# Performance work log

Hardware: AMD Instinct MI355X
Metric: run time of the kernel (lower is better)

The kernel has to match this reference:

```python
import jax, jax.numpy as jnp
import numpy as np

B, S, H, D = 4, 4096, 1024, 64

def setup_inputs() -> dict:
    key = jax.random.key(0)
    ks = jax.random.split(key, 10)
    return {
        "query": jax.random.normal(ks[0], (B, S, H), jnp.float32),
        "key": jax.random.normal(ks[1], (B, S, H), jnp.float32),
        "value": jax.random.normal(ks[2], (B, S, H), jnp.float32),
        "mask": jax.random.randint(ks[3], (B, S), 0, 2, jnp.int32),
        "Wq": jax.random.normal(ks[4], (H, D), jnp.float32) * 0.02,
        "bq": jax.random.normal(ks[5], (D,), jnp.float32) * 0.02,
        "Wk": jax.random.normal(ks[6], (H, D), jnp.float32) * 0.02,
        "bk": jax.random.normal(ks[7], (D,), jnp.float32) * 0.02,
        "Wv": jax.random.normal(ks[8], (H, D), jnp.float32) * 0.02,
        "bv": jax.random.normal(ks[9], (D,), jnp.float32) * 0.02,
    }

def reference(query, key, value, mask, Wq, bq, Wk, bk, Wv, bv):
    # single-head projections: [B,S,H] @ [H,D] -> [B,S,D]
    q = query @ Wq + bq
    k = key @ Wk + bk
    v = value @ Wv + bv
    scale = 1.0 / np.sqrt(D).astype(np.float32)
    # [B,Sq,Sk] score matrix (faithful to the unfused original)
    scores = jnp.einsum('bqd,bkd->bqk', q, k) * scale
    # mask [B,Sk] broadcast over query dim; masked positions -> -1e9
    scores = jnp.where(mask[:, None, :] == 0, jnp.float32(-1e9), scores)
    att = jax.nn.softmax(scores, axis=-1)
    # dropout prob = 0.0 -> identity
    return jnp.einsum('bqk,bkd->bqd', att, v)
```

## Files before the change

kernel.cpp:

```cpp
#include <hip/hip_runtime.h>
#include <hip/hip_bf16.h>
#include <stdint.h>


typedef __bf16 bf16;
typedef __bf16 bf16x8 __attribute__((ext_vector_type(8)));
typedef float f32x16 __attribute__((ext_vector_type(16)));

union B8 { uint4 u; bf16x8 v; uint32_t w[4]; };

#define AS1 __attribute__((address_space(1)))
#define AS3 __attribute__((address_space(3)))

__device__ __forceinline__ void async16(const void* g, void* l) {
  __builtin_amdgcn_global_load_lds((AS1 void*)(g), (AS3 void*)(l), 16, 0, 0);
}

#define KSC 0.18033688011112042f

__global__ void setup_kernel(const float* __restrict__ Wq, const float* __restrict__ Wk,
                             const float* __restrict__ Wv, const int* __restrict__ mask,
                             bf16* __restrict__ wT, float* __restrict__ biasArr)
{
  int item = blockIdx.x * 256 + threadIdx.x;
  if (item < 24576) {
    int mat = item >> 13;
    int rem = item & 8191;
    int n   = rem >> 7;
    int c   = rem & 127;
    const float* W = (mat == 0) ? Wq : (mat == 1) ? Wk : Wv;
    union { bf16 b[8]; uint4 u; } pk;
    #pragma unroll
    for (int j = 0; j < 8; ++j)
      pk.b[j] = (bf16)W[(c * 8 + j) * 64 + n];
    bf16* o = wT + mat * 65536;
    *(uint4*)(o + n * 1024 + c * 8) = pk.u;
  } else {
    int i = (item - 24576) << 2;
    const int4 m = *(const int4*)(mask + i);
    float4 b;
    b.x = m.x ? 0.0f : -1e30f;
    b.y = m.y ? 0.0f : -1e30f;
    b.z = m.z ? 0.0f : -1e30f;
    b.w = m.w ? 0.0f : -1e30f;
    *(float4*)(biasArr + i) = b;
  }
}

__global__ __launch_bounds__(64) void proj_kernel(
    const float* __restrict__ Xq, const float* __restrict__ Xk, const float* __restrict__ Xv,
    const bf16* __restrict__ wT,
    const float* __restrict__ bq, const float* __restrict__ bk, const float* __restrict__ bv,
    bf16* __restrict__ qo, bf16* __restrict__ ko, bf16* __restrict__ vTo)
{
  const int bx = blockIdx.x;
  const int mat = bx >> 9;
  const int m0 = (bx & 511) << 5;
  const float* X    = (mat == 0) ? Xq : (mat == 1) ? Xk : Xv;
  const float* bias = (mat == 0) ? bq : (mat == 1) ? bk : bv;
  const bf16* w = wT + mat * 65536;

  __shared__ __align__(16) float xbuf[2][32 * 64];
  __shared__ __align__(16) bf16 cs[32 * 64];

  const int lane = threadIdx.x;
  const int half = lane >> 5;
  const int ln = lane & 31;

  const int drow = lane >> 4;
  const int dcl  = lane & 15;

  const float* xb = X + (size_t)m0 * 1024;
  const bf16*  w0 = w + ln * 1024 + half * 8;
  const bf16*  w1 = w + (ln + 32) * 1024 + half * 8;

  float b0v = bias[ln];
  float b1v = bias[ln + 32];
  asm volatile("s_waitcnt vmcnt(0)" ::: "memory");

  #pragma unroll
  for (int i = 0; i < 8; ++i) {
    int row = i * 4 + drow;
    int sc = (dcl & 8) | ((dcl ^ (row & 7)) & 7);
    async16(xb + (size_t)row * 1024 + sc * 4, &xbuf[0][i * 256]);
  }
  uint4 wc0[4], wc1[4], wn0[4], wn1[4];
  #pragma unroll
  for (int s = 0; s < 4; ++s) {
    wc0[s] = *(const uint4*)(w0 + s * 16);
    wc1[s] = *(const uint4*)(w1 + s * 16);
  }

  f32x16 acc0 = {};
  f32x16 acc1 = {};

  for (int c = 0; c < 16; ++c) {
    if (c < 15) {
      const float* src = xb + (c + 1) * 64;
      #pragma unroll
      for (int i = 0; i < 8; ++i) {
        int row = i * 4 + drow;
        int sc = (dcl & 8) | ((dcl ^ (row & 7)) & 7);
        async16(src + (size_t)row * 1024 + sc * 4, &xbuf[(c + 1) & 1][i * 256]);
      }
      #pragma unroll
      for (int s = 0; s < 4; ++s) {
        wn0[s] = *(const uint4*)(w0 + (c + 1) * 64 + s * 16);
        wn1[s] = *(const uint4*)(w1 + (c + 1) * 64 + s * 16);
      }
      asm volatile("s_waitcnt vmcnt(16)" ::: "memory");
    } else {
      asm volatile("s_waitcnt vmcnt(0)" ::: "memory");
    }
    const float* xl = &xbuf[c & 1][0];
    #pragma unroll
    for (int s = 0; s < 4; ++s) {
      int lc = s * 4 + half * 2;
      int p0 = (lc & 8) | ((lc ^ (ln & 7)) & 7);
      int p1 = ((lc + 1) & 8) | (((lc + 1) ^ (ln & 7)) & 7);
      float4 fa = *(const float4*)(xl + ln * 64 + p0 * 4);
      float4 fb = *(const float4*)(xl + ln * 64 + p1 * 4);
      union { bf16 b[8]; bf16x8 v; } af;
      af.b[0] = (bf16)fa.x; af.b[1] = (bf16)fa.y;
      af.b[2] = (bf16)fa.z; af.b[3] = (bf16)fa.w;
      af.b[4] = (bf16)fb.x; af.b[5] = (bf16)fb.y;
      af.b[6] = (bf16)fb.z; af.b[7] = (bf16)fb.w;
      B8 wa; wa.u = wc0[s];
      B8 wb; wb.u = wc1[s];
      acc0 = __builtin_amdgcn_mfma_f32_32x32x16_bf16(af.v, wa.v, acc0, 0, 0, 0);
      acc1 = __builtin_amdgcn_mfma_f32_32x32x16_bf16(af.v, wb.v, acc1, 0, 0, 0);
    }
    #pragma unroll
    for (int s = 0; s < 4; ++s) { wc0[s] = wn0[s]; wc1[s] = wn1[s]; }
  }

  #pragma unroll
  for (int r = 0; r < 16; ++r) {
    int mrow = (r & 3) + 8 * (r >> 2) + 4 * half;
    cs[mrow * 64 + ln]      = (bf16)(acc0[r] + b0v);
    cs[mrow * 64 + ln + 32] = (bf16)(acc1[r] + b1v);
  }
  __syncthreads();

  if (mat < 2) {
    bf16* gout = (mat == 0) ? qo : ko;
    #pragma unroll
    for (int p = 0; p < 4; ++p) {
      int id = p * 64 + lane;
      int r = id >> 3;
      int c = id & 7;
      int phys = c ^ (r & 7);
      *(uint4*)(gout + (size_t)(m0 + r) * 64 + phys * 8) = *(const uint4*)(cs + r * 64 + c * 8);
    }
  } else {
    int batch = m0 >> 12;
    int sk = m0 & 4095;
    int tb = sk & ~63;
    int halfTile = (sk >> 5) & 1;
    #pragma unroll
    for (int p = 0; p < 4; ++p) {
      int id = p * 64 + lane;
      int d = id >> 2;
      int j = id & 3;
      union { bf16 b[8]; uint4 u; } pk;
      #pragma unroll
      for (int t = 0; t < 8; ++t) pk.b[t] = cs[(j * 8 + t) * 64 + d];
      int cl = halfTile * 4 + j;
      int phys = cl ^ (d & 7);
      *(uint4*)(vTo + ((size_t)batch * 64 + d) * 4096 + tb + phys * 8) = pk.u;
    }
  }
}

__global__ __launch_bounds__(256, 2) void flash_kernel(
    const bf16* __restrict__ qb, const bf16* __restrict__ kb, const bf16* __restrict__ vT,
    const float* __restrict__ biasArr, float* __restrict__ out)
{
  __shared__ __align__(16) char smem[65536];
  bf16* ksb = (bf16*)smem;
  bf16* vsb = (bf16*)(smem + 32768);

  const int tid = threadIdx.x;
  const int lane = tid & 63;
  const int wv = tid >> 6;
  const int half = lane >> 5;
  const int ln = lane & 31;

  const int batch = blockIdx.x >> 6;
  const int q0 = (blockIdx.x & 63) << 6;

  bf16x8 qf[2][4];
  const bf16* qbase = qb + ((size_t)batch * 4096 + q0) * 64;
  #pragma unroll
  for (int qk = 0; qk < 2; ++qk)
  #pragma unroll
  for (int s = 0; s < 4; ++s) {
    int qq = (qk << 5) + ln;
    int phys = (2 * s + half) ^ (qq & 7);
    B8 t; t.u = *(const uint4*)(qbase + qq * 64 + phys * 8);
    qf[qk][s] = t.v;
  }

  f32x16 acc[2][2] = {{{}, {}}, {{}, {}}};
  float den0 = 0.f, den1 = 0.f;

  bf16* kds = ksb + wv * 4096;
  bf16* vds = vsb + wv * 4096;
  const bf16* kgb = kb + (size_t)batch * 4096 * 64;
  const bf16* vgb = vT + (size_t)batch * 64 * 4096;
  const float* barr = biasArr + batch * 4096;

  for (int it = 0; it < 16; ++it) {
    const int key0 = wv * 1024 + it * 64;
    __syncthreads();
    const bf16* ksrc = kgb + (size_t)key0 * 64;
    #pragma unroll
    for (int i = 0; i < 8; ++i)
      async16((const char*)ksrc + i * 1024 + lane * 16, (char*)kds + i * 1024);
    const bf16* vsrc = vgb + key0;
    #pragma unroll
    for (int i = 0; i < 8; ++i)
      async16((const char*)vsrc + ((size_t)(i * 8 + (lane >> 3)) * 4096 + (lane & 7) * 8) * 2,
              (char*)vds + i * 1024);
    __syncthreads();

    #pragma unroll
    for (int st = 0; st < 2; ++st) {
      f32x16 s0 = {};
      f32x16 s1 = {};
      #pragma unroll
      for (int s = 0; s < 4; ++s) {
        int key = (st << 5) + ln;
        B8 af; af.u = *(const uint4*)(kds + key * 64 + (((2 * s + half) ^ (key & 7)) << 3));
        s0 = __builtin_amdgcn_mfma_f32_32x32x16_bf16(af.v, qf[0][s], s0, 0, 0, 0);
        s1 = __builtin_amdgcn_mfma_f32_32x32x16_bf16(af.v, qf[1][s], s1, 0, 0, 0);
      }
      float bb[16];
      #pragma unroll
      for (int g = 0; g < 4; ++g)
        *(float4*)&bb[4 * g] = *(const float4*)(barr + key0 + (st << 5) + 8 * g + (half << 2));
      uint32_t pk0[8], pk1[8];
      #pragma unroll
      for (int i = 0; i < 8; ++i) {
        float a0 = __builtin_amdgcn_exp2f(fmaf(s0[2 * i],     KSC, bb[2 * i]));
        float a1 = __builtin_amdgcn_exp2f(fmaf(s0[2 * i + 1], KSC, bb[2 * i + 1]));
        float c0 = __builtin_amdgcn_exp2f(fmaf(s1[2 * i],     KSC, bb[2 * i]));
        float c1 = __builtin_amdgcn_exp2f(fmaf(s1[2 * i + 1], KSC, bb[2 * i + 1]));
        den0 += a0 + a1;
        den1 += c0 + c1;
        union { bf16 b[2]; uint32_t u; } u0, u1;
        u0.b[0] = (bf16)a0; u0.b[1] = (bf16)a1;
        u1.b[0] = (bf16)c0; u1.b[1] = (bf16)c1;
        pk0[i] = u0.u; pk1[i] = u1.u;
      }
      uint32_t xp0[8], xp1[8];
      #pragma unroll
      for (int i = 0; i < 8; ++i) {
        xp0[i] = (uint32_t)__shfl_xor((int)pk0[i], 32);
        xp1[i] = (uint32_t)__shfl_xor((int)pk1[i], 32);
      }
      #pragma unroll
      for (int t = 0; t < 2; ++t) {
        B8 p0f, p1f;
        p0f.w[0] = half ? xp0[4 * t + 2] : pk0[4 * t];
        p0f.w[1] = half ? xp0[4 * t + 3] : pk0[4 * t + 1];
        p0f.w[2] = half ? pk0[4 * t + 2] : xp0[4 * t];
        p0f.w[3] = half ? pk0[4 * t + 3] : xp0[4 * t + 1];
        p1f.w[0] = half ? xp1[4 * t + 2] : pk1[4 * t];
        p1f.w[1] = half ? xp1[4 * t + 3] : pk1[4 * t + 1];
        p1f.w[2] = half ? pk1[4 * t + 2] : xp1[4 * t];
        p1f.w[3] = half ? pk1[4 * t + 3] : xp1[4 * t + 1];
        #pragma unroll
        for (int dh = 0; dh < 2; ++dh) {
          int d = (dh << 5) + ln;
          B8 vf; vf.u = *(const uint4*)(vds + d * 64 +
                          ((((st << 2) + (t << 1) + half) ^ (d & 7)) << 3));
          acc[0][dh] = __builtin_amdgcn_mfma_f32_32x32x16_bf16(vf.v, p0f.v, acc[0][dh], 0, 0, 0);
          acc[1][dh] = __builtin_amdgcn_mfma_f32_32x32x16_bf16(vf.v, p1f.v, acc[1][dh], 0, 0, 0);
        }
      }
    }
  }

  den0 += __shfl_xor(den0, 32);
  den1 += __shfl_xor(den1, 32);

  float* nb = (float*)smem;
  float* dn = (float*)(smem + 34816);

  __syncthreads();
  if (wv >= 2) {
    float* mynb = nb + (wv - 2) * 4352;
    #pragma unroll
    for (int qk = 0; qk < 2; ++qk)
    #pragma unroll
    for (int dh = 0; dh < 2; ++dh)
    #pragma unroll
    for (int g = 0; g < 4; ++g) {
      int q = (qk << 5) + ln;
      int d = 8 * g + (half << 2) + (dh << 5);
      f32x16 a = acc[qk][dh];
      *(float4*)(mynb + q * 68 + d) = make_float4(a[4*g], a[4*g+1], a[4*g+2], a[4*g+3]);
    }
    if (half == 0) {
      dn[(wv - 2) * 64 + ln]      = den0;
      dn[(wv - 2) * 64 + 32 + ln] = den1;
    }
  }
  __syncthreads();
  if (wv < 2) {
    float* pb = nb + wv * 4352;
    #pragma unroll
    for (int qk = 0; qk < 2; ++qk)
    #pragma unroll
    for (int dh = 0; dh < 2; ++dh)
    #pragma unroll
    for (int g = 0; g < 4; ++g) {
      int q = (qk << 5) + ln;
      int d = 8 * g + (half << 2) + (dh << 5);
      float4 t = *(const float4*)(pb + q * 68 + d);
      acc[qk][dh][4*g+0] += t.x; acc[qk][dh][4*g+1] += t.y;
      acc[qk][dh][4*g+2] += t.z; acc[qk][dh][4*g+3] += t.w;
    }
    den0 += dn[wv * 64 + ln];
    den1 += dn[wv * 64 + 32 + ln];
  }
  __syncthreads();
  if (wv < 2) {
    float* mynb = nb + wv * 4352;
    #pragma unroll
    for (int qk = 0; qk < 2; ++qk)
    #pragma unroll
    for (int dh = 0; dh < 2; ++dh)
    #pragma unroll
    for (int g = 0; g < 4; ++g) {
      int q = (qk << 5) + ln;
      int d = 8 * g + (half << 2) + (dh << 5);
      f32x16 a = acc[qk][dh];
      *(float4*)(mynb + q * 68 + d) = make_float4(a[4*g], a[4*g+1], a[4*g+2], a[4*g+3]);
    }
    if (half == 0) {
      dn[wv * 64 + ln]      = den0;
      dn[wv * 64 + 32 + ln] = den1;
    }
  }
  __syncthreads();
  #pragma unroll
  for (int p = 0; p < 4; ++p) {
    int i = p * 256 + tid;
    int qq = i >> 4;
    int d4 = (i & 15) << 2;
    float4 A = *(const float4*)(nb + qq * 68 + d4);
    float4 Bv = *(const float4*)(nb + 4352 + qq * 68 + d4);
    float dd = dn[qq] + dn[64 + qq];
    float inv = 1.0f / dd;
    float4 o = make_float4((A.x + Bv.x) * inv, (A.y + Bv.y) * inv,
                           (A.z + Bv.z) * inv, (A.w + Bv.w) * inv);
    *(float4*)(out + ((size_t)batch * 4096 + q0 + qq) * 64 + d4) = o;
  }
}

extern "C" void kernel_launch(void* const* d_in, const int* in_sizes, int n_in,
                              void* d_out, int out_size, void* d_ws, size_t ws_size,
                              hipStream_t stream)
{
  const float* query = (const float*)d_in[0];
  const float* key   = (const float*)d_in[1];
  const float* value = (const float*)d_in[2];
  const int*   mask  = (const int*)d_in[3];
  const float* Wq    = (const float*)d_in[4];
  const float* bq    = (const float*)d_in[5];
  const float* Wk    = (const float*)d_in[6];
  const float* bk    = (const float*)d_in[7];
  const float* Wv    = (const float*)d_in[8];
  const float* bv    = (const float*)d_in[9];
  float* out = (float*)d_out;

  bf16* qb = (bf16*)d_ws;
  bf16* kb = qb + 1048576;
  bf16* vT = kb + 1048576;
  bf16* wT = vT + 1048576;
  float* biasArr = (float*)((char*)d_ws + 3 * 2097152 + 393216);

  setup_kernel<<<112, 256, 0, stream>>>(Wq, Wk, Wv, mask, wT, biasArr);
  proj_kernel<<<1536, 64, 0, stream>>>(query, key, value, wT, bq, bk, bv, qb, kb, vT);
  flash_kernel<<<256, 256, 0, stream>>>(qb, kb, vT, biasArr, out);
}
```

Before: 267.8 us.

## Split projection block across two waves, each computing half the output columns

The projection kernel now runs 128 threads per block instead of 64. Each wave computes one 32-column half of the 64-wide output, with its own accumulator and weight registers. The two waves share the async X tile loads and synchronise with barriers around each chunk. The goal is to halve per-wave work and register pressure and to raise latency hiding for this memory-bound stage, at the cost of two extra barriers per chunk.

```diff
diff --git a/kernel.cpp b/kernel.cpp
--- a/kernel.cpp
+++ b/kernel.cpp
@@ -47,7 +47,7 @@
   }
 }
 
-__global__ __launch_bounds__(64) void proj_kernel(
+__global__ __launch_bounds__(128) void proj_kernel(
     const float* __restrict__ Xq, const float* __restrict__ Xk, const float* __restrict__ Xv,
     const bf16* __restrict__ wT,
     const float* __restrict__ bq, const float* __restrict__ bk, const float* __restrict__ bv,
@@ -63,55 +63,55 @@
   __shared__ __align__(16) float xbuf[2][32 * 64];
   __shared__ __align__(16) bf16 cs[32 * 64];
 
-  const int lane = threadIdx.x;
+  const int tid  = threadIdx.x;
+  const int wv   = tid >> 6;
+  const int lane = tid & 63;
   const int half = lane >> 5;
-  const int ln = lane & 31;
+  const int ln   = lane & 31;
 
   const int drow = lane >> 4;
   const int dcl  = lane & 15;
 
   const float* xb = X + (size_t)m0 * 1024;
-  const bf16*  w0 = w + ln * 1024 + half * 8;
-  const bf16*  w1 = w + (ln + 32) * 1024 + half * 8;
-
-  float b0v = bias[ln];
-  float b1v = bias[ln + 32];
+  const bf16*  w0 = w + ((wv << 5) + ln) * 1024 + half * 8;
+
+  float b0v = bias[(wv << 5) + ln];
   asm volatile("s_waitcnt vmcnt(0)" ::: "memory");
 
   #pragma unroll
-  for (int i = 0; i < 8; ++i) {
-    int row = i * 4 + drow;
+  for (int i = 0; i < 4; ++i) {
+    int ii = (wv << 2) + i;
+    int row = ii * 4 + drow;
     int sc = (dcl & 8) | ((dcl ^ (row & 7)) & 7);
-    async16(xb + (size_t)row * 1024 + sc * 4, &xbuf[0][i * 256]);
-  }
-  uint4 wc0[4], wc1[4], wn0[4], wn1[4];
-  #pragma unroll
-  for (int s = 0; s < 4; ++s) {
-    wc0[s] = *(const uint4*)(w0 + s * 16);
-    wc1[s] = *(const uint4*)(w1 + s * 16);
-  }
-
-  f32x16 acc0 = {};
-  f32x16 acc1 = {};
+    async16(xb + (size_t)row * 1024 + sc * 4, &xbuf[0][ii * 256]);
+  }
+  uint4 wc[4], wn[4];
+  #pragma unroll
+  for (int s = 0; s < 4; ++s)
+    wc[s] = *(const uint4*)(w0 + s * 16);
+
+  f32x16 acc = {};
 
   for (int c = 0; c < 16; ++c) {
     if (c < 15) {
       const float* src = xb + (c + 1) * 64;
       #pragma unroll
-      for (int i = 0; i < 8; ++i) {
-        int row = i * 4 + drow;
+      for (int i = 0; i < 4; ++i) {
+        int ii = (wv << 2) + i;
+        int row = ii * 4 + drow;
         int sc = (dcl & 8) | ((dcl ^ (row & 7)) & 7);
-        async16(src + (size_t)row * 1024 + sc * 4, &xbuf[(c + 1) & 1][i * 256]);
-      }
-      #pragma unroll
-      for (int s = 0; s < 4; ++s) {
-        wn0[s] = *(const uint4*)(w0 + (c + 1) * 64 + s * 16);
-        wn1[s] = *(const uint4*)(w1 + (c + 1) * 64 + s * 16);
-      }
-      asm volatile("s_waitcnt vmcnt(16)" ::: "memory");
+        async16(src + (size_t)row * 1024 + sc * 4, &xbuf[(c + 1) & 1][ii * 256]);
+      }
+      #pragma unroll
+      for (int s = 0; s < 4; ++s)
+        wn[s] = *(const uint4*)(w0 + (c + 1) * 64 + s * 16);
+      asm volatile("s_waitcnt vmcnt(8)" ::: "memory");
     } else {
       asm volatile("s_waitcnt vmcnt(0)" ::: "memory");
     }
+    __builtin_amdgcn_s_barrier();
+    asm volatile("" ::: "memory");
+
     const float* xl = &xbuf[c & 1][0];
     #pragma unroll
     for (int s = 0; s < 4; ++s) {
@@ -125,28 +125,27 @@
       af.b[2] = (bf16)fa.z; af.b[3] = (bf16)fa.w;
       af.b[4] = (bf16)fb.x; af.b[5] = (bf16)fb.y;
       af.b[6] = (bf16)fb.z; af.b[7] = (bf16)fb.w;
-      B8 wa; wa.u = wc0[s];
-      B8 wb; wb.u = wc1[s];
-      acc0 = __builtin_amdgcn_mfma_f32_32x32x16_bf16(af.v, wa.v, acc0, 0, 0, 0);
-      acc1 = __builtin_amdgcn_mfma_f32_32x32x16_bf16(af.v, wb.v, acc1, 0, 0, 0);
-    }
-    #pragma unroll
-    for (int s = 0; s < 4; ++s) { wc0[s] = wn0[s]; wc1[s] = wn1[s]; }
+      B8 wa; wa.u = wc[s];
+      acc = __builtin_amdgcn_mfma_f32_32x32x16_bf16(af.v, wa.v, acc, 0, 0, 0);
+    }
+    asm volatile("s_waitcnt lgkmcnt(0)" ::: "memory");
+    __builtin_amdgcn_s_barrier();
+    #pragma unroll
+    for (int s = 0; s < 4; ++s) wc[s] = wn[s];
   }
 
   #pragma unroll
   for (int r = 0; r < 16; ++r) {
     int mrow = (r & 3) + 8 * (r >> 2) + 4 * half;
-    cs[mrow * 64 + ln]      = (bf16)(acc0[r] + b0v);
-    cs[mrow * 64 + ln + 32] = (bf16)(acc1[r] + b1v);
+    cs[mrow * 64 + (wv << 5) + ln] = (bf16)(acc[r] + b0v);
   }
   __syncthreads();
 
   if (mat < 2) {
     bf16* gout = (mat == 0) ? qo : ko;
     #pragma unroll
-    for (int p = 0; p < 4; ++p) {
-      int id = p * 64 + lane;
+    for (int p = 0; p < 2; ++p) {
+      int id = p * 128 + tid;
       int r = id >> 3;
       int c = id & 7;
       int phys = c ^ (r & 7);
@@ -158,8 +157,8 @@
     int tb = sk & ~63;
     int halfTile = (sk >> 5) & 1;
     #pragma unroll
-    for (int p = 0; p < 4; ++p) {
-      int id = p * 64 + lane;
+    for (int p = 0; p < 2; ++p) {
+      int id = p * 128 + tid;
       int d = id >> 2;
       int j = id & 3;
       union { bf16 b[8]; uint4 u; } pk;
@@ -383,6 +382,6 @@
   float* biasArr = (float*)((char*)d_ws + 3 * 2097152 + 393216);
 
   setup_kernel<<<112, 256, 0, stream>>>(Wq, Wk, Wv, mask, wT, biasArr);
-  proj_kernel<<<1536, 64, 0, stream>>>(query, key, value, wT, bq, bk, bv, qb, kb, vT);
+  proj_kernel<<<1536, 128, 0, stream>>>(query, key, value, wT, bq, bk, bv, qb, kb, vT);
   flash_kernel<<<256, 256, 0, stream>>>(qb, kb, vT, biasArr, out);
 }
```

Result: no change. 264.9 us (-1.1%).
